# Performance work log

Measured on AMD Instinct MI355X. Metric: run time of the kernel, lower is better.

Reference implementation:

```python
import jax, jax.numpy as jnp
import numpy as np

N = 8192
IN_F = 128
OUT_F = 64
ALPHA = 0.2  # LeakyReLU slope
NEG_FILL = -9e15


def setup_inputs() -> dict:
    key = jax.random.key(0)
    k1, k2, k3, k4 = jax.random.split(key, 4)
    inp = jax.random.normal(k1, (N, IN_F), dtype=jnp.float32)
    adj = jax.random.randint(k2, (N, N), 0, 2, dtype=jnp.int32)
    W = jax.random.normal(k3, (IN_F, OUT_F), dtype=jnp.float32) * (1.414 / np.sqrt(IN_F))
    a = jax.random.normal(k4, (2 * OUT_F, 1), dtype=jnp.float32) * 0.1
    return {"input": inp, "adj": adj, "W": W, "a": a}


def reference(input, adj, W, a):
    # h: [N, F]
    h = input @ W
    a1 = a[:OUT_F, 0]   # [F]
    a2 = a[OUT_F:, 0]   # [F]
    # e_ij = leakyrelu(h_i . a1 + h_j . a2)  -- avoids O(N^2 * 2F) concat
    f1 = h @ a1  # [N]
    f2 = h @ a2  # [N]
    e = jax.nn.leaky_relu(f1[:, None] + f2[None, :], negative_slope=ALPHA)  # [N, N]
    scores = jnp.where(adj > 0, e, NEG_FILL)
    attn = jax.nn.softmax(scores, axis=1)  # [N, N]
    h_prime = attn @ h  # [N, F]
    return jax.nn.elu(h_prime)
```

## Files before the change

### kernel.cpp

```cpp
#include <hip/hip_runtime.h>

#define N 8192
#define IN_F 128
#define OUT_F 64
#define ALPHA 0.2f

#define RB 32
#define JT 128
#define TB 512
#define JC 8

typedef int          iv4    __attribute__((ext_vector_type(4)));
typedef unsigned int uv4    __attribute__((ext_vector_type(4)));
typedef unsigned int uv2    __attribute__((ext_vector_type(2)));
typedef __bf16       bf16x8 __attribute__((ext_vector_type(8)));
typedef float        f32x4  __attribute__((ext_vector_type(4)));

__device__ __forceinline__ unsigned short f2bf(float x) {
  unsigned u = __float_as_uint(x);
  u += 0x7fffu + ((u >> 16) & 1u);
  return (unsigned short)(u >> 16);
}
__device__ __forceinline__ float bf2f(unsigned short b) {
  return __uint_as_float(((unsigned)b) << 16);
}

__global__ __launch_bounds__(256) void gat_prep(
    const float* __restrict__ input, const float* __restrict__ W,
    const float* __restrict__ a,
    unsigned short* __restrict__ ht, float* __restrict__ f1,
    float* __restrict__ f2, float* __restrict__ bmax)
{
  __shared__ float Ws[IN_F * OUT_F];
  __shared__ float ins[8][IN_F];
  __shared__ __align__(16) unsigned short Hts[OUT_F][8];
  __shared__ float bm[4];
  int t = threadIdx.x;

  const float4* W4 = (const float4*)W;
  float4* Ws4 = (float4*)Ws;
#pragma unroll
  for (int k = 0; k < 8; ++k) Ws4[t + 256 * k] = W4[t + 256 * k];

  int row0 = blockIdx.x * 8;
  const float4* in4 = (const float4*)(input + (size_t)row0 * IN_F);
  ((float4*)&ins[0][0])[t] = in4[t];
  __syncthreads();

  int w = t >> 6, o = t & 63;
  float a1v = a[o], a2v = a[OUT_F + o];
  float pmax = -3.4e38f;

#pragma unroll
  for (int p = 0; p < 2; ++p) {
    int r = p * 4 + w;
    int i = row0 + r;
    const float4* iv = (const float4*)&ins[r][0];
    float acc = 0.f;
#pragma unroll
    for (int k4 = 0; k4 < 32; ++k4) {
      float4 v = iv[k4];
      acc += v.x * Ws[(k4 * 4 + 0) * OUT_F + o];
      acc += v.y * Ws[(k4 * 4 + 1) * OUT_F + o];
      acc += v.z * Ws[(k4 * 4 + 2) * OUT_F + o];
      acc += v.w * Ws[(k4 * 4 + 3) * OUT_F + o];
    }
    Hts[o][r] = f2bf(acc);
    float p1 = acc * a1v, p2 = acc * a2v;
#pragma unroll
    for (int m = 32; m >= 1; m >>= 1) {
      p1 += __shfl_xor(p1, m, 64);
      p2 += __shfl_xor(p2, m, 64);
    }
    pmax = fmaxf(pmax, p2);
    if (o == 0) {
      f1[i] = p1;
      f2[i] = p2;
    }
  }
  if (o == 0) bm[w] = pmax;
  __syncthreads();
  if (t < 64) {
    uv4 v = *(const uv4*)&Hts[t][0];
    *(uv4*)&ht[(size_t)t * N + row0] = v;
  }
  if (t == 0)
    bmax[blockIdx.x] = fmaxf(fmaxf(bm[0], bm[1]), fmaxf(bm[2], bm[3]));
}

__global__ __launch_bounds__(TB) void gat_part(
    const int* __restrict__ adj, const unsigned short* __restrict__ ht,
    const float* __restrict__ f1, const float* __restrict__ f2,
    const float* __restrict__ bmax,
    float* __restrict__ num, float* __restrict__ den, int jcc)
{
  __shared__ __align__(16) unsigned short HtS[2][OUT_F * JT];
  __shared__ __align__(16) unsigned short PS[2][RB * JT];
  __shared__ float F1s[RB];
  __shared__ float Ms[RB];
  __shared__ float gm[8];

  int t = threadIdx.x;
  int ib = blockIdx.x & 255;
  int jc = blockIdx.x >> 8;
  int i0 = ib * RB;
  int T = (N / JT) / jcc;

  {
    float v = fmaxf(bmax[t], bmax[t + 512]);
#pragma unroll
    for (int m = 32; m >= 1; m >>= 1) v = fmaxf(v, __shfl_xor(v, m, 64));
    if ((t & 63) == 0) gm[t >> 6] = v;
  }
  __syncthreads();
  if (t < RB) {
    float g = gm[0];
#pragma unroll
    for (int k = 1; k < 8; ++k) g = fmaxf(g, gm[k]);
    float f1v = f1[i0 + t];
    F1s[t] = f1v;
    float e = f1v + g;
    Ms[t] = e > 0.f ? e : ALPHA * e;
  }

  int jq = t & 31, rp = t >> 5;
  int so = t >> 3, sc = t & 7;
  int w = t >> 6, l = t & 63;
  int m0 = (w & 1) * 16, n0 = (w >> 1) * 16;
  int arow = m0 + (l & 15);
  int bcol = n0 + (l & 15);
  int kg = (l >> 4) * 16;
  unsigned aswz = (unsigned)((arow & 7) << 4);
  unsigned bswz = (unsigned)((bcol & 7) << 4);
  unsigned sswz = (unsigned)((so & 7) << 4);
  unsigned pswz = (unsigned)((rp & 7) << 4);

  float lsum0 = 0.f, lsum1 = 0.f;
  f32x4 acc = {0.f, 0.f, 0.f, 0.f};

  int jt0 = jc * T, jt1 = (jc + 1) * T;
  const int* arow0 = adj + (size_t)(i0 + rp) * N;
  const int* arow1 = adj + (size_t)(i0 + rp + 16) * N;

  iv4 av0 = __builtin_nontemporal_load((const iv4*)(arow0 + jt0 * JT) + jq);
  iv4 av1 = __builtin_nontemporal_load((const iv4*)(arow1 + jt0 * JT) + jq);
  __syncthreads();

  int buf = 0;
  for (int jt = jt0; jt < jt1; ++jt) {
    int j0 = jt * JT;
    char* HtSb = (char*)&HtS[buf][0];
    char* PSb = (char*)&PS[buf][0];

    {
      const unsigned short* src = ht + (size_t)so * N + j0 + sc * 8;
      uv4 h0 = *(const uv4*)(src);
      uv4 h1 = *(const uv4*)(src + 64);
      *(uv4*)(HtSb + (((unsigned)(so * 256 + sc * 16)) ^ sswz)) = h0;
      *(uv4*)(HtSb + (((unsigned)(so * 256 + 128 + sc * 16)) ^ sswz)) = h1;
    }

    {
      float4 fv = *(const float4*)(f2 + j0 + jq * 4);
      float e; float4 pv; uv2 w2;

      float f1v = F1s[rp], mv = Ms[rp];
      e = f1v + fv.x; e = e > 0.f ? e : ALPHA * e; pv.x = (av0.x > 0) ? __expf(e - mv) : 0.f;
      e = f1v + fv.y; e = e > 0.f ? e : ALPHA * e; pv.y = (av0.y > 0) ? __expf(e - mv) : 0.f;
      e = f1v + fv.z; e = e > 0.f ? e : ALPHA * e; pv.z = (av0.z > 0) ? __expf(e - mv) : 0.f;
      e = f1v + fv.w; e = e > 0.f ? e : ALPHA * e; pv.w = (av0.w > 0) ? __expf(e - mv) : 0.f;
      unsigned short b0 = f2bf(pv.x), b1 = f2bf(pv.y), b2 = f2bf(pv.z), b3 = f2bf(pv.w);
      lsum0 += (bf2f(b0) + bf2f(b1)) + (bf2f(b2) + bf2f(b3));
      w2.x = (unsigned)b0 | ((unsigned)b1 << 16);
      w2.y = (unsigned)b2 | ((unsigned)b3 << 16);
      *(uv2*)(PSb + (((unsigned)(rp * 256 + jq * 8)) ^ pswz)) = w2;

      f1v = F1s[rp + 16]; mv = Ms[rp + 16];
      e = f1v + fv.x; e = e > 0.f ? e : ALPHA * e; pv.x = (av1.x > 0) ? __expf(e - mv) : 0.f;
      e = f1v + fv.y; e = e > 0.f ? e : ALPHA * e; pv.y = (av1.y > 0) ? __expf(e - mv) : 0.f;
      e = f1v + fv.z; e = e > 0.f ? e : ALPHA * e; pv.z = (av1.z > 0) ? __expf(e - mv) : 0.f;
      e = f1v + fv.w; e = e > 0.f ? e : ALPHA * e; pv.w = (av1.w > 0) ? __expf(e - mv) : 0.f;
      b0 = f2bf(pv.x); b1 = f2bf(pv.y); b2 = f2bf(pv.z); b3 = f2bf(pv.w);
      lsum1 += (bf2f(b0) + bf2f(b1)) + (bf2f(b2) + bf2f(b3));
      w2.x = (unsigned)b0 | ((unsigned)b1 << 16);
      w2.y = (unsigned)b2 | ((unsigned)b3 << 16);
      *(uv2*)(PSb + (((unsigned)((rp + 16) * 256 + jq * 8)) ^ pswz)) = w2;
    }

    if (jt + 1 < jt1) {
      av0 = __builtin_nontemporal_load((const iv4*)(arow0 + (jt + 1) * JT) + jq);
      av1 = __builtin_nontemporal_load((const iv4*)(arow1 + (jt + 1) * JT) + jq);
    }
    __syncthreads();

#pragma unroll
    for (int ks = 0; ks < 4; ++ks) {
      bf16x8 a8 = __builtin_bit_cast(bf16x8,
          *(const uv4*)(PSb + (((unsigned)(arow * 256 + ks * 64 + kg)) ^ aswz)));
      bf16x8 b8 = __builtin_bit_cast(bf16x8,
          *(const uv4*)(HtSb + (((unsigned)(bcol * 256 + ks * 64 + kg)) ^ bswz)));
      acc = __builtin_amdgcn_mfma_f32_16x16x32_bf16(a8, b8, acc, 0, 0, 0);
    }
    buf ^= 1;
  }

#pragma unroll
  for (int m = 16; m >= 1; m >>= 1) {
    lsum0 += __shfl_xor(lsum0, m, 64);
    lsum1 += __shfl_xor(lsum1, m, 64);
  }
  if ((t & 31) == 0) {
    den[(size_t)jc * N + i0 + rp] = lsum0;
    den[(size_t)jc * N + i0 + rp + 16] = lsum1;
  }

  int crow = i0 + m0 + ((l >> 4) << 2);
  float* np = num + ((size_t)jc * N + crow) * OUT_F + n0 + (l & 15);
  np[0 * OUT_F] = acc[0];
  np[1 * OUT_F] = acc[1];
  np[2 * OUT_F] = acc[2];
  np[3 * OUT_F] = acc[3];
}

__global__ __launch_bounds__(256) void gat_reduce(
    const unsigned short* __restrict__ ht, const float* __restrict__ num,
    const float* __restrict__ den, float* __restrict__ out, int jcc)
{
  int t = threadIdx.x;
  int i = blockIdx.x * 16 + (t >> 4);
  int o4 = t & 15;

  float d = 0.f;
  for (int c = 0; c < jcc; ++c) d += den[(size_t)c * N + i];

  float a0 = 0.f, a1 = 0.f, a2 = 0.f, a3 = 0.f;
  for (int c = 0; c < jcc; ++c) {
    float4 v = *(const float4*)&num[(((size_t)c * N) + i) * OUT_F + o4 * 4];
    a0 += v.x; a1 += v.y; a2 += v.z; a3 += v.w;
  }

  if (d <= 0.f) {
    a0 = a1 = a2 = a3 = 0.f;
    for (int j = 0; j < N; ++j) {
      a0 += bf2f(ht[(size_t)(o4 * 4 + 0) * N + j]);
      a1 += bf2f(ht[(size_t)(o4 * 4 + 1) * N + j]);
      a2 += bf2f(ht[(size_t)(o4 * 4 + 2) * N + j]);
      a3 += bf2f(ht[(size_t)(o4 * 4 + 3) * N + j]);
    }
    d = (float)N;
  }
  float inv = 1.f / d;
  a0 *= inv; a1 *= inv; a2 *= inv; a3 *= inv;
  float4 r4;
  r4.x = a0 > 0.f ? a0 : expm1f(a0);
  r4.y = a1 > 0.f ? a1 : expm1f(a1);
  r4.z = a2 > 0.f ? a2 : expm1f(a2);
  r4.w = a3 > 0.f ? a3 : expm1f(a3);
  *(float4*)&out[(size_t)i * OUT_F + o4 * 4] = r4;
}

extern "C" void kernel_launch(void* const* d_in, const int* in_sizes, int n_in,
                              void* d_out, int out_size, void* d_ws, size_t ws_size,
                              hipStream_t stream) {
  const float* input = (const float*)d_in[0];
  const int*   adj   = (const int*)d_in[1];
  const float* W     = (const float*)d_in[2];
  const float* a     = (const float*)d_in[3];
  float* out = (float*)d_out;

  unsigned short* ht = (unsigned short*)d_ws;
  float* f1 = (float*)(ht + (size_t)N * OUT_F);
  float* f2 = f1 + N;
  float* bmax = f2 + N;
  float* den = bmax + N / 8;
  float* num = den + (size_t)JC * N;
  size_t need = (size_t)((char*)(num + (size_t)JC * N * OUT_F) - (char*)d_ws);

  int jcc = (ws_size >= need) ? JC : 1;

  gat_prep<<<N / 8, 256, 0, stream>>>(input, W, a, ht, f1, f2, bmax);
  gat_part<<<jcc * (N / RB), TB, 0, stream>>>(adj, ht, f1, f2, bmax, num, den, jcc);
  gat_reduce<<<N / 16, 256, 0, stream>>>(ht, num, den, out, jcc);
}
```

Baseline: 84.71 us.

## Load ht operands directly to registers, deepen adj prefetch, remap P-tile threads

Removes the shared-memory staging of the ht (B operand) tile: each lane now loads its MFMA B fragments straight from global memory into registers. Threads are remapped so each handles one row and 8 consecutive columns, writing one 16-byte P-tile store, and adj loads are prefetched two tiles ahead with a manually unrolled two-tile loop. Launch bounds add a min-blocks hint of 4. This cuts LDS traffic and shared-memory footprint but adds uncoalesced-ish global reads of ht per wave and relies on the tile count per chunk being even.

New measurement: 133.2 us. 1.57x slower.

```diff
diff --git a/kernel.cpp b/kernel.cpp
--- a/kernel.cpp
+++ b/kernel.cpp
@@ -12,7 +12,6 @@
 
 typedef int          iv4    __attribute__((ext_vector_type(4)));
 typedef unsigned int uv4    __attribute__((ext_vector_type(4)));
-typedef unsigned int uv2    __attribute__((ext_vector_type(2)));
 typedef __bf16       bf16x8 __attribute__((ext_vector_type(8)));
 typedef float        f32x4  __attribute__((ext_vector_type(4)));
 
@@ -88,13 +87,12 @@
     bmax[blockIdx.x] = fmaxf(fmaxf(bm[0], bm[1]), fmaxf(bm[2], bm[3]));
 }
 
-__global__ __launch_bounds__(TB) void gat_part(
+__global__ __launch_bounds__(TB, 4) void gat_part(
     const int* __restrict__ adj, const unsigned short* __restrict__ ht,
     const float* __restrict__ f1, const float* __restrict__ f2,
     const float* __restrict__ bmax,
     float* __restrict__ num, float* __restrict__ den, int jcc)
 {
-  __shared__ __align__(16) unsigned short HtS[2][OUT_F * JT];
   __shared__ __align__(16) unsigned short PS[2][RB * JT];
   __shared__ float F1s[RB];
   __shared__ float Ms[RB];
@@ -122,97 +120,91 @@
     float e = f1v + g;
     Ms[t] = e > 0.f ? e : ALPHA * e;
   }
-
-  int jq = t & 31, rp = t >> 5;
-  int so = t >> 3, sc = t & 7;
+  __syncthreads();
+
+  int r = t >> 4, jq8 = (t & 15) * 8;
+  float f1v = F1s[r], mv = Ms[r];
+  unsigned pswz = (unsigned)(r * 256 + (t & 15) * 16) ^ (unsigned)((r & 7) << 4);
+
   int w = t >> 6, l = t & 63;
   int m0 = (w & 1) * 16, n0 = (w >> 1) * 16;
   int arow = m0 + (l & 15);
   int bcol = n0 + (l & 15);
   int kg = (l >> 4) * 16;
   unsigned aswz = (unsigned)((arow & 7) << 4);
-  unsigned bswz = (unsigned)((bcol & 7) << 4);
-  unsigned sswz = (unsigned)((so & 7) << 4);
-  unsigned pswz = (unsigned)((rp & 7) << 4);
-
-  float lsum0 = 0.f, lsum1 = 0.f;
+  const unsigned short* bbase = ht + (size_t)bcol * N + (l >> 4) * 8;
+
+  float lsum = 0.f;
   f32x4 acc = {0.f, 0.f, 0.f, 0.f};
 
   int jt0 = jc * T, jt1 = (jc + 1) * T;
-  const int* arow0 = adj + (size_t)(i0 + rp) * N;
-  const int* arow1 = adj + (size_t)(i0 + rp + 16) * N;
-
-  iv4 av0 = __builtin_nontemporal_load((const iv4*)(arow0 + jt0 * JT) + jq);
-  iv4 av1 = __builtin_nontemporal_load((const iv4*)(arow1 + jt0 * JT) + jq);
-  __syncthreads();
+  const int* ar = adj + (size_t)(i0 + r) * N + jq8;
+
+  iv4 avA0 = __builtin_nontemporal_load((const iv4*)(ar + jt0 * JT));
+  iv4 avA1 = __builtin_nontemporal_load((const iv4*)(ar + jt0 * JT) + 1);
+  iv4 avB0 = __builtin_nontemporal_load((const iv4*)(ar + (jt0 + 1) * JT));
+  iv4 avB1 = __builtin_nontemporal_load((const iv4*)(ar + (jt0 + 1) * JT) + 1);
 
   int buf = 0;
-  for (int jt = jt0; jt < jt1; ++jt) {
-    int j0 = jt * JT;
-    char* HtSb = (char*)&HtS[buf][0];
-    char* PSb = (char*)&PS[buf][0];
-
-    {
-      const unsigned short* src = ht + (size_t)so * N + j0 + sc * 8;
-      uv4 h0 = *(const uv4*)(src);
-      uv4 h1 = *(const uv4*)(src + 64);
-      *(uv4*)(HtSb + (((unsigned)(so * 256 + sc * 16)) ^ sswz)) = h0;
-      *(uv4*)(HtSb + (((unsigned)(so * 256 + 128 + sc * 16)) ^ sswz)) = h1;
-    }
-
-    {
-      float4 fv = *(const float4*)(f2 + j0 + jq * 4);
-      float e; float4 pv; uv2 w2;
-
-      float f1v = F1s[rp], mv = Ms[rp];
-      e = f1v + fv.x; e = e > 0.f ? e : ALPHA * e; pv.x = (av0.x > 0) ? __expf(e - mv) : 0.f;
-      e = f1v + fv.y; e = e > 0.f ? e : ALPHA * e; pv.y = (av0.y > 0) ? __expf(e - mv) : 0.f;
-      e = f1v + fv.z; e = e > 0.f ? e : ALPHA * e; pv.z = (av0.z > 0) ? __expf(e - mv) : 0.f;
-      e = f1v + fv.w; e = e > 0.f ? e : ALPHA * e; pv.w = (av0.w > 0) ? __expf(e - mv) : 0.f;
-      unsigned short b0 = f2bf(pv.x), b1 = f2bf(pv.y), b2 = f2bf(pv.z), b3 = f2bf(pv.w);
-      lsum0 += (bf2f(b0) + bf2f(b1)) + (bf2f(b2) + bf2f(b3));
-      w2.x = (unsigned)b0 | ((unsigned)b1 << 16);
-      w2.y = (unsigned)b2 | ((unsigned)b3 << 16);
-      *(uv2*)(PSb + (((unsigned)(rp * 256 + jq * 8)) ^ pswz)) = w2;
-
-      f1v = F1s[rp + 16]; mv = Ms[rp + 16];
-      e = f1v + fv.x; e = e > 0.f ? e : ALPHA * e; pv.x = (av1.x > 0) ? __expf(e - mv) : 0.f;
-      e = f1v + fv.y; e = e > 0.f ? e : ALPHA * e; pv.y = (av1.y > 0) ? __expf(e - mv) : 0.f;
-      e = f1v + fv.z; e = e > 0.f ? e : ALPHA * e; pv.z = (av1.z > 0) ? __expf(e - mv) : 0.f;
-      e = f1v + fv.w; e = e > 0.f ? e : ALPHA * e; pv.w = (av1.w > 0) ? __expf(e - mv) : 0.f;
-      b0 = f2bf(pv.x); b1 = f2bf(pv.y); b2 = f2bf(pv.z); b3 = f2bf(pv.w);
-      lsum1 += (bf2f(b0) + bf2f(b1)) + (bf2f(b2) + bf2f(b3));
-      w2.x = (unsigned)b0 | ((unsigned)b1 << 16);
-      w2.y = (unsigned)b2 | ((unsigned)b3 << 16);
-      *(uv2*)(PSb + (((unsigned)((rp + 16) * 256 + jq * 8)) ^ pswz)) = w2;
-    }
-
-    if (jt + 1 < jt1) {
-      av0 = __builtin_nontemporal_load((const iv4*)(arow0 + (jt + 1) * JT) + jq);
-      av1 = __builtin_nontemporal_load((const iv4*)(arow1 + (jt + 1) * JT) + jq);
-    }
-    __syncthreads();
-
-#pragma unroll
-    for (int ks = 0; ks < 4; ++ks) {
-      bf16x8 a8 = __builtin_bit_cast(bf16x8,
-          *(const uv4*)(PSb + (((unsigned)(arow * 256 + ks * 64 + kg)) ^ aswz)));
-      bf16x8 b8 = __builtin_bit_cast(bf16x8,
-          *(const uv4*)(HtSb + (((unsigned)(bcol * 256 + ks * 64 + kg)) ^ bswz)));
-      acc = __builtin_amdgcn_mfma_f32_16x16x32_bf16(a8, b8, acc, 0, 0, 0);
-    }
-    buf ^= 1;
-  }
-
-#pragma unroll
-  for (int m = 16; m >= 1; m >>= 1) {
-    lsum0 += __shfl_xor(lsum0, m, 64);
-    lsum1 += __shfl_xor(lsum1, m, 64);
-  }
-  if ((t & 31) == 0) {
-    den[(size_t)jc * N + i0 + rp] = lsum0;
-    den[(size_t)jc * N + i0 + rp + 16] = lsum1;
-  }
+
+#define TILE_BODY(JTI, AV0, AV1)                                              \
+  {                                                                           \
+    int j0 = (JTI) * JT;                                                      \
+    char* PSb = (char*)&PS[buf][0];                                           \
+                                       \
+    const unsigned short* bp = bbase + j0;                                    \
+    uv4 b0 = *(const uv4*)(bp);                                               \
+    uv4 b1 = *(const uv4*)(bp + 32);                                          \
+    uv4 b2 = *(const uv4*)(bp + 64);                                          \
+    uv4 b3 = *(const uv4*)(bp + 96);                                          \
+                      \
+    float4 fv0 = *(const float4*)(f2 + j0 + jq8);                             \
+    float4 fv1 = *(const float4*)(f2 + j0 + jq8 + 4);                         \
+    float e; uv4 w4;                                                          \
+    unsigned short c0, c1, c2, c3;                                            \
+    e = f1v + fv0.x; e = e > 0.f ? e : ALPHA * e; c0 = (AV0.x > 0) ? f2bf(__expf(e - mv)) : 0; \
+    e = f1v + fv0.y; e = e > 0.f ? e : ALPHA * e; c1 = (AV0.y > 0) ? f2bf(__expf(e - mv)) : 0; \
+    e = f1v + fv0.z; e = e > 0.f ? e : ALPHA * e; c2 = (AV0.z > 0) ? f2bf(__expf(e - mv)) : 0; \
+    e = f1v + fv0.w; e = e > 0.f ? e : ALPHA * e; c3 = (AV0.w > 0) ? f2bf(__expf(e - mv)) : 0; \
+    lsum += (bf2f(c0) + bf2f(c1)) + (bf2f(c2) + bf2f(c3));                    \
+    w4.x = (unsigned)c0 | ((unsigned)c1 << 16);                               \
+    w4.y = (unsigned)c2 | ((unsigned)c3 << 16);                               \
+    e = f1v + fv1.x; e = e > 0.f ? e : ALPHA * e; c0 = (AV1.x > 0) ? f2bf(__expf(e - mv)) : 0; \
+    e = f1v + fv1.y; e = e > 0.f ? e : ALPHA * e; c1 = (AV1.y > 0) ? f2bf(__expf(e - mv)) : 0; \
+    e = f1v + fv1.z; e = e > 0.f ? e : ALPHA * e; c2 = (AV1.z > 0) ? f2bf(__expf(e - mv)) : 0; \
+    e = f1v + fv1.w; e = e > 0.f ? e : ALPHA * e; c3 = (AV1.w > 0) ? f2bf(__expf(e - mv)) : 0; \
+    lsum += (bf2f(c0) + bf2f(c1)) + (bf2f(c2) + bf2f(c3));                    \
+    w4.z = (unsigned)c0 | ((unsigned)c1 << 16);                               \
+    w4.w = (unsigned)c2 | ((unsigned)c3 << 16);                               \
+    *(uv4*)(PSb + pswz) = w4;                                                 \
+                    \
+    if ((JTI) + 2 < jt1) {                                                    \
+      AV0 = __builtin_nontemporal_load((const iv4*)(ar + ((JTI) + 2) * JT));  \
+      AV1 = __builtin_nontemporal_load((const iv4*)(ar + ((JTI) + 2) * JT) + 1); \
+    }                                                                         \
+    __syncthreads();          \
+    bf16x8 a8;                                                                \
+    a8 = __builtin_bit_cast(bf16x8, *(const uv4*)(PSb + (((unsigned)(arow * 256 + 0 * 64 + kg)) ^ aswz))); \
+    acc = __builtin_amdgcn_mfma_f32_16x16x32_bf16(a8, __builtin_bit_cast(bf16x8, b0), acc, 0, 0, 0); \
+    a8 = __builtin_bit_cast(bf16x8, *(const uv4*)(PSb + (((unsigned)(arow * 256 + 1 * 64 + kg)) ^ aswz))); \
+    acc = __builtin_amdgcn_mfma_f32_16x16x32_bf16(a8, __builtin_bit_cast(bf16x8, b1), acc, 0, 0, 0); \
+    a8 = __builtin_bit_cast(bf16x8, *(const uv4*)(PSb + (((unsigned)(arow * 256 + 2 * 64 + kg)) ^ aswz))); \
+    acc = __builtin_amdgcn_mfma_f32_16x16x32_bf16(a8, __builtin_bit_cast(bf16x8, b2), acc, 0, 0, 0); \
+    a8 = __builtin_bit_cast(bf16x8, *(const uv4*)(PSb + (((unsigned)(arow * 256 + 3 * 64 + kg)) ^ aswz))); \
+    acc = __builtin_amdgcn_mfma_f32_16x16x32_bf16(a8, __builtin_bit_cast(bf16x8, b3), acc, 0, 0, 0); \
+    buf ^= 1;                                                                 \
+  }
+
+  for (int jt = jt0; jt < jt1; jt += 2) {
+    TILE_BODY(jt, avA0, avA1);
+    TILE_BODY(jt + 1, avB0, avB1);
+  }
+#undef TILE_BODY
+
+#pragma unroll
+  for (int m = 1; m <= 8; m <<= 1) lsum += __shfl_xor(lsum, m, 64);
+  if ((l & 15) == 0)
+    den[(size_t)jc * N + i0 + (w << 2) + (l >> 4)] = lsum;
 
   int crow = i0 + m0 + ((l >> 4) << 2);
   float* np = num + ((size_t)jc * N + crow) * OUT_F + n0 + (l & 15);
```

## Store h in MFMA fragment layout and load B operands directly from global

Applied to the files above, without the earlier changes.

The transposed bf16 feature matrix is now written by the prep kernel in a blocked layout of 32-column chunks, so each MFMA lane can load its B operand fragment straight from global memory instead of staging it through LDS. This drops the per-tile HtS shared buffer, its stores, and its reads. Each thread also now handles one row and eight adjacent columns of the probability tile, writing 16-byte LDS stores and loading F1/M once outside the loop. The kernel gets a launch-bounds occupancy hint. The trade-off is redundant global and L2 traffic for h across waves and blocks, plus more register pressure.

Measured after the change: 104.4 us. +23.2%, slower.

```diff
diff --git a/kernel.cpp b/kernel.cpp
--- a/kernel.cpp
+++ b/kernel.cpp
@@ -12,7 +12,6 @@
 
 typedef int          iv4    __attribute__((ext_vector_type(4)));
 typedef unsigned int uv4    __attribute__((ext_vector_type(4)));
-typedef unsigned int uv2    __attribute__((ext_vector_type(2)));
 typedef __bf16       bf16x8 __attribute__((ext_vector_type(8)));
 typedef float        f32x4  __attribute__((ext_vector_type(4)));
 
@@ -25,10 +24,12 @@
   return __uint_as_float(((unsigned)b) << 16);
 }
 
+#define HTF_OFF(J, COL) (((size_t)((J) >> 5) * (OUT_F * 32)) + (COL) * 32 + ((J) & 31))
+
 __global__ __launch_bounds__(256) void gat_prep(
     const float* __restrict__ input, const float* __restrict__ W,
     const float* __restrict__ a,
-    unsigned short* __restrict__ ht, float* __restrict__ f1,
+    unsigned short* __restrict__ htf, float* __restrict__ f1,
     float* __restrict__ f2, float* __restrict__ bmax)
 {
   __shared__ float Ws[IN_F * OUT_F];
@@ -82,19 +83,18 @@
   __syncthreads();
   if (t < 64) {
     uv4 v = *(const uv4*)&Hts[t][0];
-    *(uv4*)&ht[(size_t)t * N + row0] = v;
+    *(uv4*)&htf[HTF_OFF(row0, t)] = v;
   }
   if (t == 0)
     bmax[blockIdx.x] = fmaxf(fmaxf(bm[0], bm[1]), fmaxf(bm[2], bm[3]));
 }
 
-__global__ __launch_bounds__(TB) void gat_part(
-    const int* __restrict__ adj, const unsigned short* __restrict__ ht,
+__global__ __launch_bounds__(TB, 8) void gat_part(
+    const int* __restrict__ adj, const unsigned short* __restrict__ htf,
     const float* __restrict__ f1, const float* __restrict__ f2,
     const float* __restrict__ bmax,
     float* __restrict__ num, float* __restrict__ den, int jcc)
 {
-  __shared__ __align__(16) unsigned short HtS[2][OUT_F * JT];
   __shared__ __align__(16) unsigned short PS[2][RB * JT];
   __shared__ float F1s[RB];
   __shared__ float Ms[RB];
@@ -122,97 +122,87 @@
     float e = f1v + g;
     Ms[t] = e > 0.f ? e : ALPHA * e;
   }
-
-  int jq = t & 31, rp = t >> 5;
-  int so = t >> 3, sc = t & 7;
+  __syncthreads();
+
+  int r = t >> 4, jq8 = (t & 15) * 8;
+  float f1v = F1s[r], mv = Ms[r];
+  unsigned pswz = (unsigned)(r * 256) +
+                  (((unsigned)((t & 15) * 16)) ^ (unsigned)((r & 7) << 4));
+
   int w = t >> 6, l = t & 63;
   int m0 = (w & 1) * 16, n0 = (w >> 1) * 16;
   int arow = m0 + (l & 15);
-  int bcol = n0 + (l & 15);
   int kg = (l >> 4) * 16;
   unsigned aswz = (unsigned)((arow & 7) << 4);
-  unsigned bswz = (unsigned)((bcol & 7) << 4);
-  unsigned sswz = (unsigned)((so & 7) << 4);
-  unsigned pswz = (unsigned)((rp & 7) << 4);
-
-  float lsum0 = 0.f, lsum1 = 0.f;
+  unsigned abase = (unsigned)(arow * 256);
+  const unsigned short* bbase = htf + (size_t)(n0 + (l & 15)) * 32 + (l >> 4) * 8;
+
+  float lsum = 0.f;
   f32x4 acc = {0.f, 0.f, 0.f, 0.f};
 
   int jt0 = jc * T, jt1 = (jc + 1) * T;
-  const int* arow0 = adj + (size_t)(i0 + rp) * N;
-  const int* arow1 = adj + (size_t)(i0 + rp + 16) * N;
-
-  iv4 av0 = __builtin_nontemporal_load((const iv4*)(arow0 + jt0 * JT) + jq);
-  iv4 av1 = __builtin_nontemporal_load((const iv4*)(arow1 + jt0 * JT) + jq);
-  __syncthreads();
+  const int* ar = adj + (size_t)(i0 + r) * N + jq8;
+
+  iv4 av0 = __builtin_nontemporal_load((const iv4*)(ar + jt0 * JT));
+  iv4 av1 = __builtin_nontemporal_load((const iv4*)(ar + jt0 * JT) + 1);
 
   int buf = 0;
   for (int jt = jt0; jt < jt1; ++jt) {
     int j0 = jt * JT;
-    char* HtSb = (char*)&HtS[buf][0];
     char* PSb = (char*)&PS[buf][0];
 
+    const unsigned short* bp = bbase + (size_t)(j0 >> 5) * (OUT_F * 32);
+    uv4 b0 = *(const uv4*)(bp);
+    uv4 b1 = *(const uv4*)(bp + OUT_F * 32);
+    uv4 b2 = *(const uv4*)(bp + OUT_F * 64);
+    uv4 b3 = *(const uv4*)(bp + OUT_F * 96);
+
     {
-      const unsigned short* src = ht + (size_t)so * N + j0 + sc * 8;
-      uv4 h0 = *(const uv4*)(src);
-      uv4 h1 = *(const uv4*)(src + 64);
-      *(uv4*)(HtSb + (((unsigned)(so * 256 + sc * 16)) ^ sswz)) = h0;
-      *(uv4*)(HtSb + (((unsigned)(so * 256 + 128 + sc * 16)) ^ sswz)) = h1;
-    }
+      float4 fv0 = *(const float4*)(f2 + j0 + jq8);
+      float4 fv1 = *(const float4*)(f2 + j0 + jq8 + 4);
+      float e; uv4 w4;
+      unsigned short c0, c1, c2, c3;
+      e = f1v + fv0.x; e = e > 0.f ? e : ALPHA * e; c0 = (av0.x > 0) ? f2bf(__expf(e - mv)) : 0;
+      e = f1v + fv0.y; e = e > 0.f ? e : ALPHA * e; c1 = (av0.y > 0) ? f2bf(__expf(e - mv)) : 0;
+      e = f1v + fv0.z; e = e > 0.f ? e : ALPHA * e; c2 = (av0.z > 0) ? f2bf(__expf(e - mv)) : 0;
+      e = f1v + fv0.w; e = e > 0.f ? e : ALPHA * e; c3 = (av0.w > 0) ? f2bf(__expf(e - mv)) : 0;
+      lsum += (bf2f(c0) + bf2f(c1)) + (bf2f(c2) + bf2f(c3));
+      w4.x = (unsigned)c0 | ((unsigned)c1 << 16);
+      w4.y = (unsigned)c2 | ((unsigned)c3 << 16);
+      e = f1v + fv1.x; e = e > 0.f ? e : ALPHA * e; c0 = (av1.x > 0) ? f2bf(__expf(e - mv)) : 0;
+      e = f1v + fv1.y; e = e > 0.f ? e : ALPHA * e; c1 = (av1.y > 0) ? f2bf(__expf(e - mv)) : 0;
+      e = f1v + fv1.z; e = e > 0.f ? e : ALPHA * e; c2 = (av1.z > 0) ? f2bf(__expf(e - mv)) : 0;
+      e = f1v + fv1.w; e = e > 0.f ? e : ALPHA * e; c3 = (av1.w > 0) ? f2bf(__expf(e - mv)) : 0;
+      lsum += (bf2f(c0) + bf2f(c1)) + (bf2f(c2) + bf2f(c3));
+      w4.z = (unsigned)c0 | ((unsigned)c1 << 16);
+      w4.w = (unsigned)c2 | ((unsigned)c3 << 16);
+      *(uv4*)(PSb + pswz) = w4;
+    }
+
+    if (jt + 1 < jt1) {
+      av0 = __builtin_nontemporal_load((const iv4*)(ar + (jt + 1) * JT));
+      av1 = __builtin_nontemporal_load((const iv4*)(ar + (jt + 1) * JT) + 1);
+    }
+    __syncthreads();
 
     {
-      float4 fv = *(const float4*)(f2 + j0 + jq * 4);
-      float e; float4 pv; uv2 w2;
-
-      float f1v = F1s[rp], mv = Ms[rp];
-      e = f1v + fv.x; e = e > 0.f ? e : ALPHA * e; pv.x = (av0.x > 0) ? __expf(e - mv) : 0.f;
-      e = f1v + fv.y; e = e > 0.f ? e : ALPHA * e; pv.y = (av0.y > 0) ? __expf(e - mv) : 0.f;
-      e = f1v + fv.z; e = e > 0.f ? e : ALPHA * e; pv.z = (av0.z > 0) ? __expf(e - mv) : 0.f;
-      e = f1v + fv.w; e = e > 0.f ? e : ALPHA * e; pv.w = (av0.w > 0) ? __expf(e - mv) : 0.f;
-      unsigned short b0 = f2bf(pv.x), b1 = f2bf(pv.y), b2 = f2bf(pv.z), b3 = f2bf(pv.w);
-      lsum0 += (bf2f(b0) + bf2f(b1)) + (bf2f(b2) + bf2f(b3));
-      w2.x = (unsigned)b0 | ((unsigned)b1 << 16);
-      w2.y = (unsigned)b2 | ((unsigned)b3 << 16);
-      *(uv2*)(PSb + (((unsigned)(rp * 256 + jq * 8)) ^ pswz)) = w2;
-
-      f1v = F1s[rp + 16]; mv = Ms[rp + 16];
-      e = f1v + fv.x; e = e > 0.f ? e : ALPHA * e; pv.x = (av1.x > 0) ? __expf(e - mv) : 0.f;
-      e = f1v + fv.y; e = e > 0.f ? e : ALPHA * e; pv.y = (av1.y > 0) ? __expf(e - mv) : 0.f;
-      e = f1v + fv.z; e = e > 0.f ? e : ALPHA * e; pv.z = (av1.z > 0) ? __expf(e - mv) : 0.f;
-      e = f1v + fv.w; e = e > 0.f ? e : ALPHA * e; pv.w = (av1.w > 0) ? __expf(e - mv) : 0.f;
-      b0 = f2bf(pv.x); b1 = f2bf(pv.y); b2 = f2bf(pv.z); b3 = f2bf(pv.w);
-      lsum1 += (bf2f(b0) + bf2f(b1)) + (bf2f(b2) + bf2f(b3));
-      w2.x = (unsigned)b0 | ((unsigned)b1 << 16);
-      w2.y = (unsigned)b2 | ((unsigned)b3 << 16);
-      *(uv2*)(PSb + (((unsigned)((rp + 16) * 256 + jq * 8)) ^ pswz)) = w2;
-    }
-
-    if (jt + 1 < jt1) {
-      av0 = __builtin_nontemporal_load((const iv4*)(arow0 + (jt + 1) * JT) + jq);
-      av1 = __builtin_nontemporal_load((const iv4*)(arow1 + (jt + 1) * JT) + jq);
-    }
-    __syncthreads();
-
-#pragma unroll
-    for (int ks = 0; ks < 4; ++ks) {
-      bf16x8 a8 = __builtin_bit_cast(bf16x8,
-          *(const uv4*)(PSb + (((unsigned)(arow * 256 + ks * 64 + kg)) ^ aswz)));
-      bf16x8 b8 = __builtin_bit_cast(bf16x8,
-          *(const uv4*)(HtSb + (((unsigned)(bcol * 256 + ks * 64 + kg)) ^ bswz)));
-      acc = __builtin_amdgcn_mfma_f32_16x16x32_bf16(a8, b8, acc, 0, 0, 0);
+      bf16x8 a8;
+      a8 = __builtin_bit_cast(bf16x8, *(const uv4*)(PSb + (abase + ((0 * 64 + kg) ^ aswz))));
+      acc = __builtin_amdgcn_mfma_f32_16x16x32_bf16(a8, __builtin_bit_cast(bf16x8, b0), acc, 0, 0, 0);
+      a8 = __builtin_bit_cast(bf16x8, *(const uv4*)(PSb + (abase + ((1 * 64 + kg) ^ aswz))));
+      acc = __builtin_amdgcn_mfma_f32_16x16x32_bf16(a8, __builtin_bit_cast(bf16x8, b1), acc, 0, 0, 0);
+      a8 = __builtin_bit_cast(bf16x8, *(const uv4*)(PSb + (abase + ((2 * 64 + kg) ^ aswz))));
+      acc = __builtin_amdgcn_mfma_f32_16x16x32_bf16(a8, __builtin_bit_cast(bf16x8, b2), acc, 0, 0, 0);
+      a8 = __builtin_bit_cast(bf16x8, *(const uv4*)(PSb + (abase + ((3 * 64 + kg) ^ aswz))));
+      acc = __builtin_amdgcn_mfma_f32_16x16x32_bf16(a8, __builtin_bit_cast(bf16x8, b3), acc, 0, 0, 0);
     }
     buf ^= 1;
   }
 
 #pragma unroll
-  for (int m = 16; m >= 1; m >>= 1) {
-    lsum0 += __shfl_xor(lsum0, m, 64);
-    lsum1 += __shfl_xor(lsum1, m, 64);
-  }
-  if ((t & 31) == 0) {
-    den[(size_t)jc * N + i0 + rp] = lsum0;
-    den[(size_t)jc * N + i0 + rp + 16] = lsum1;
-  }
+  for (int m = 1; m <= 8; m <<= 1) lsum += __shfl_xor(lsum, m, 64);
+  if ((l & 15) == 0)
+    den[(size_t)jc * N + i0 + (w << 2) + (l >> 4)] = lsum;
 
   int crow = i0 + m0 + ((l >> 4) << 2);
   float* np = num + ((size_t)jc * N + crow) * OUT_F + n0 + (l & 15);
@@ -223,7 +213,7 @@
 }
 
 __global__ __launch_bounds__(256) void gat_reduce(
-    const unsigned short* __restrict__ ht, const float* __restrict__ num,
+    const unsigned short* __restrict__ htf, const float* __restrict__ num,
     const float* __restrict__ den, float* __restrict__ out, int jcc)
 {
   int t = threadIdx.x;
@@ -242,10 +232,10 @@
   if (d <= 0.f) {
     a0 = a1 = a2 = a3 = 0.f;
     for (int j = 0; j < N; ++j) {
-      a0 += bf2f(ht[(size_t)(o4 * 4 + 0) * N + j]);
-      a1 += bf2f(ht[(size_t)(o4 * 4 + 1) * N + j]);
-      a2 += bf2f(ht[(size_t)(o4 * 4 + 2) * N + j]);
-      a3 += bf2f(ht[(size_t)(o4 * 4 + 3) * N + j]);
+      a0 += bf2f(htf[HTF_OFF(j, o4 * 4 + 0)]);
+      a1 += bf2f(htf[HTF_OFF(j, o4 * 4 + 1)]);
+      a2 += bf2f(htf[HTF_OFF(j, o4 * 4 + 2)]);
+      a3 += bf2f(htf[HTF_OFF(j, o4 * 4 + 3)]);
     }
     d = (float)N;
   }
@@ -268,8 +258,8 @@
   const float* a     = (const float*)d_in[3];
   float* out = (float*)d_out;
 
-  unsigned short* ht = (unsigned short*)d_ws;
-  float* f1 = (float*)(ht + (size_t)N * OUT_F);
+  unsigned short* htf = (unsigned short*)d_ws;
+  float* f1 = (float*)(htf + (size_t)N * OUT_F);
   float* f2 = f1 + N;
   float* bmax = f2 + N;
   float* den = bmax + N / 8;
@@ -278,7 +268,7 @@
 
   int jcc = (ws_size >= need) ? JC : 1;
 
-  gat_prep<<<N / 8, 256, 0, stream>>>(input, W, a, ht, f1, f2, bmax);
-  gat_part<<<jcc * (N / RB), TB, 0, stream>>>(adj, ht, f1, f2, bmax, num, den, jcc);
-  gat_reduce<<<N / 16, 256, 0, stream>>>(ht, num, den, out, jcc);
-}
+  gat_prep<<<N / 8, 256, 0, stream>>>(input, W, a, htf, f1, f2, bmax);
+  gat_part<<<jcc * (N / RB), TB, 0, stream>>>(adj, htf, f1, f2, bmax, num, den, jcc);
+  gat_reduce<<<N / 16, 256, 0, stream>>>(htf, num, den, out, jcc);
+}
```

## Pre-pack adjacency matrix into bitmask before attention kernel

Applied to the files above, without the earlier changes.

Adds a pass that converts the int32 adjacency matrix into a 1-bit-per-entry mask using wavefront ballots. The main attention kernel then reads one byte of mask instead of 16-byte int vectors per thread, which cuts its global traffic. The full adjacency matrix must still be read once by the new pass, so the aim is to move streaming traffic out of the compute-heavy kernel. This adds a kernel launch and workspace for the mask.

Result: slower. 143.7 us (+69.7%).

```diff
diff --git a/kernel.cpp b/kernel.cpp
--- a/kernel.cpp
+++ b/kernel.cpp
@@ -23,6 +23,21 @@
 }
 __device__ __forceinline__ float bf2f(unsigned short b) {
   return __uint_as_float(((unsigned)b) << 16);
+}
+
+__global__ __launch_bounds__(256) void gat_pack(
+    const int* __restrict__ adj, unsigned long long* __restrict__ pb)
+{
+  size_t g = (size_t)blockIdx.x * 4 + (threadIdx.x >> 6);
+  int lane = threadIdx.x & 63;
+  const int* p = adj + g * 128 * 64 + lane;
+  unsigned long long* q = pb + g * 128;
+#pragma unroll 4
+  for (int it = 0; it < 128; ++it) {
+    int v = p[(size_t)it * 64];
+    unsigned long long m = __ballot(v > 0);
+    if (lane == 0) q[it] = m;
+  }
 }
 
 __global__ __launch_bounds__(256) void gat_prep(
@@ -89,7 +104,7 @@
 }
 
 __global__ __launch_bounds__(TB) void gat_part(
-    const int* __restrict__ adj, const unsigned short* __restrict__ ht,
+    const unsigned char* __restrict__ pb, const unsigned short* __restrict__ ht,
     const float* __restrict__ f1, const float* __restrict__ f2,
     const float* __restrict__ bmax,
     float* __restrict__ num, float* __restrict__ den, int jcc)
@@ -139,11 +154,12 @@
   f32x4 acc = {0.f, 0.f, 0.f, 0.f};
 
   int jt0 = jc * T, jt1 = (jc + 1) * T;
-  const int* arow0 = adj + (size_t)(i0 + rp) * N;
-  const int* arow1 = adj + (size_t)(i0 + rp + 16) * N;
-
-  iv4 av0 = __builtin_nontemporal_load((const iv4*)(arow0 + jt0 * JT) + jq);
-  iv4 av1 = __builtin_nontemporal_load((const iv4*)(arow1 + jt0 * JT) + jq);
+  const unsigned char* pr0 = pb + (size_t)(i0 + rp) * (N / 8) + (jq >> 1);
+  const unsigned char* pr1 = pb + (size_t)(i0 + rp + 16) * (N / 8) + (jq >> 1);
+  int nsh = (jq & 1) * 4;
+
+  unsigned bm0 = pr0[jt0 * (JT / 8)];
+  unsigned bm1 = pr1[jt0 * (JT / 8)];
   __syncthreads();
 
   int buf = 0;
@@ -163,23 +179,22 @@
     {
       float4 fv = *(const float4*)(f2 + j0 + jq * 4);
       float e; float4 pv; uv2 w2;
-
+      unsigned s0 = bm0 >> nsh, s1 = bm1 >> nsh;
       float f1v = F1s[rp], mv = Ms[rp];
-      e = f1v + fv.x; e = e > 0.f ? e : ALPHA * e; pv.x = (av0.x > 0) ? __expf(e - mv) : 0.f;
-      e = f1v + fv.y; e = e > 0.f ? e : ALPHA * e; pv.y = (av0.y > 0) ? __expf(e - mv) : 0.f;
-      e = f1v + fv.z; e = e > 0.f ? e : ALPHA * e; pv.z = (av0.z > 0) ? __expf(e - mv) : 0.f;
-      e = f1v + fv.w; e = e > 0.f ? e : ALPHA * e; pv.w = (av0.w > 0) ? __expf(e - mv) : 0.f;
+      e = f1v + fv.x; e = e > 0.f ? e : ALPHA * e; pv.x = (s0 & 1u) ? __expf(e - mv) : 0.f;
+      e = f1v + fv.y; e = e > 0.f ? e : ALPHA * e; pv.y = (s0 & 2u) ? __expf(e - mv) : 0.f;
+      e = f1v + fv.z; e = e > 0.f ? e : ALPHA * e; pv.z = (s0 & 4u) ? __expf(e - mv) : 0.f;
+      e = f1v + fv.w; e = e > 0.f ? e : ALPHA * e; pv.w = (s0 & 8u) ? __expf(e - mv) : 0.f;
       unsigned short b0 = f2bf(pv.x), b1 = f2bf(pv.y), b2 = f2bf(pv.z), b3 = f2bf(pv.w);
       lsum0 += (bf2f(b0) + bf2f(b1)) + (bf2f(b2) + bf2f(b3));
       w2.x = (unsigned)b0 | ((unsigned)b1 << 16);
       w2.y = (unsigned)b2 | ((unsigned)b3 << 16);
       *(uv2*)(PSb + (((unsigned)(rp * 256 + jq * 8)) ^ pswz)) = w2;
-
       f1v = F1s[rp + 16]; mv = Ms[rp + 16];
-      e = f1v + fv.x; e = e > 0.f ? e : ALPHA * e; pv.x = (av1.x > 0) ? __expf(e - mv) : 0.f;
-      e = f1v + fv.y; e = e > 0.f ? e : ALPHA * e; pv.y = (av1.y > 0) ? __expf(e - mv) : 0.f;
-      e = f1v + fv.z; e = e > 0.f ? e : ALPHA * e; pv.z = (av1.z > 0) ? __expf(e - mv) : 0.f;
-      e = f1v + fv.w; e = e > 0.f ? e : ALPHA * e; pv.w = (av1.w > 0) ? __expf(e - mv) : 0.f;
+      e = f1v + fv.x; e = e > 0.f ? e : ALPHA * e; pv.x = (s1 & 1u) ? __expf(e - mv) : 0.f;
+      e = f1v + fv.y; e = e > 0.f ? e : ALPHA * e; pv.y = (s1 & 2u) ? __expf(e - mv) : 0.f;
+      e = f1v + fv.z; e = e > 0.f ? e : ALPHA * e; pv.z = (s1 & 4u) ? __expf(e - mv) : 0.f;
+      e = f1v + fv.w; e = e > 0.f ? e : ALPHA * e; pv.w = (s1 & 8u) ? __expf(e - mv) : 0.f;
       b0 = f2bf(pv.x); b1 = f2bf(pv.y); b2 = f2bf(pv.z); b3 = f2bf(pv.w);
       lsum1 += (bf2f(b0) + bf2f(b1)) + (bf2f(b2) + bf2f(b3));
       w2.x = (unsigned)b0 | ((unsigned)b1 << 16);
@@ -188,8 +203,8 @@
     }
 
     if (jt + 1 < jt1) {
-      av0 = __builtin_nontemporal_load((const iv4*)(arow0 + (jt + 1) * JT) + jq);
-      av1 = __builtin_nontemporal_load((const iv4*)(arow1 + (jt + 1) * JT) + jq);
+      bm0 = pr0[(jt + 1) * (JT / 8)];
+      bm1 = pr1[(jt + 1) * (JT / 8)];
     }
     __syncthreads();
 
@@ -272,13 +287,15 @@
   float* f1 = (float*)(ht + (size_t)N * OUT_F);
   float* f2 = f1 + N;
   float* bmax = f2 + N;
-  float* den = bmax + N / 8;
+  unsigned long long* pbw = (unsigned long long*)(bmax + N / 8);
+  float* den = (float*)(pbw + (size_t)N * N / 64);
   float* num = den + (size_t)JC * N;
   size_t need = (size_t)((char*)(num + (size_t)JC * N * OUT_F) - (char*)d_ws);
 
   int jcc = (ws_size >= need) ? JC : 1;
 
+  gat_pack<<<2048, 256, 0, stream>>>(adj, pbw);
   gat_prep<<<N / 8, 256, 0, stream>>>(input, W, a, ht, f1, f2, bmax);
-  gat_part<<<jcc * (N / RB), TB, 0, stream>>>(adj, ht, f1, f2, bmax, num, den, jcc);
+  gat_part<<<jcc * (N / RB), TB, 0, stream>>>((const unsigned char*)pbw, ht, f1, f2, bmax, num, den, jcc);
   gat_reduce<<<N / 16, 256, 0, stream>>>(ht, num, den, out, jcc);
 }
```
